# Kernel tuning notes

Measured on AMD Instinct MI355X. Metric: run time of the kernel, lower is better.

## Reference

```python
import jax, jax.numpy as jnp
import numpy as np

SAMPLE_RATE = 48000.0
WIN_SIZE = 512   # also the FFT size (nfft = win_size in forward)
HOP_SIZE = 256   # win_size // 2, COLA with Hann
B = 128
NUM_FREQ_PTS = 96000  # 2 s RIR at 48 kHz


def _hann(n):
    # torch.hann_window default is periodic: 0.5*(1 - cos(2*pi*k/n))
    k = jnp.arange(n, dtype=jnp.float32)
    return 0.5 * (1.0 - jnp.cos(2.0 * jnp.pi * k / n))


def _stft(x, win, nfft, hop):
    # x: [B, L] real. center=False, onesided=True, not normalized.
    L = x.shape[-1]
    pad = (-L) % hop  # pad to multiple of hop, as in get_stft_torch
    if pad:
        x = jnp.pad(x, ((0, 0), (0, pad)))
    T = (x.shape[-1] - nfft) // hop + 1  # number of frames
    idx = hop * jnp.arange(T)[:, None] + jnp.arange(nfft)[None, :]  # [T, nfft]
    frames = x[:, idx] * win  # [B, T, nfft]
    return jnp.fft.rfft(frames, n=nfft, axis=-1)  # [B, T, F], F = nfft//2 + 1


def _edr_db(S):
    # S: [B, T, F] complex. EDR[m] = sum_{t>=m} |S[t]|^2  -> reverse cumsum (O(T)).
    P = jnp.abs(S) ** 2  # [B, T, F]
    edr = jnp.flip(jnp.cumsum(jnp.flip(P, axis=1), axis=1), axis=1)
    return 10.0 * jnp.log10(edr)  # db(..., is_squared=True)


def reference(target_re, target_im, ach_re, ach_im):
    n = target_re.shape[-1]
    target_rir = jnp.fft.irfft(target_re + 1j * target_im, n=n)
    ach_rir = jnp.fft.irfft(ach_re + 1j * ach_im, n=n)
    win = _hann(WIN_SIZE)
    S_t = _stft(target_rir, win, WIN_SIZE, HOP_SIZE)
    S_a = _stft(ach_rir, win, WIN_SIZE, HOP_SIZE)
    edr_t = _edr_db(S_t)
    edr_a = _edr_db(S_a)
    return jnp.sum(jnp.abs(edr_t - edr_a)) / jnp.sum(jnp.abs(edr_t))


def setup_inputs() -> dict:
    key = jax.random.key(0)
    k1, k2, k3, k4 = jax.random.split(key, 4)
    shape = (B, NUM_FREQ_PTS)
    return {
        "target_re": jax.random.normal(k1, shape, dtype=jnp.float32),
        "target_im": jax.random.normal(k2, shape, dtype=jnp.float32),
        "ach_re": jax.random.normal(k3, shape, dtype=jnp.float32),
        "ach_im": jax.random.normal(k4, shape, dtype=jnp.float32),
    }
```

## Files before the change

### kernel.cpp

```cpp
#include <hip/hip_runtime.h>
#include <math.h>

#define BATCH   128
#define NFREQ   96000
#define M_HALF  48000
#define NFRAMES 374
#define NBINS   257
#define PPITCH  258
#define NG      11
#define GLEN    34
#define FPW     4

#define CS1 246
#define CS2 206

#define PI_D 3.14159265358979323846

#define WAVE_SYNC() __asm__ volatile("s_waitcnt lgkmcnt(0)" ::: "memory")

__device__ __forceinline__ float2 cmulf(float2 a, float2 b) {
  return make_float2(a.x * b.x - a.y * b.y, a.x * b.y + a.y * b.x);
}

__device__ __forceinline__ void bfly4(float2 z0, float2 z1, float2 z2, float2 z3,
                                      float2& o0, float2& o1, float2& o2, float2& o3) {
  float2 e0 = make_float2(z0.x + z2.x, z0.y + z2.y);
  float2 e1 = make_float2(z0.x - z2.x, z0.y - z2.y);
  float2 e2 = make_float2(z1.x + z3.x, z1.y + z3.y);
  float2 e3 = make_float2(z1.x - z3.x, z1.y - z3.y);
  o0 = make_float2(e0.x + e2.x, e0.y + e2.y);
  o2 = make_float2(e0.x - e2.x, e0.y - e2.y);
  o1 = make_float2(e1.x + e3.y, e1.y - e3.x);
  o3 = make_float2(e1.x - e3.y, e1.y + e3.x);
}

__device__ __forceinline__ void bfly4i(float2 z0, float2 z1, float2 z2, float2 z3,
                                       float2& o0, float2& o1, float2& o2, float2& o3) {
  float2 e0 = make_float2(z0.x + z2.x, z0.y + z2.y);
  float2 e1 = make_float2(z0.x - z2.x, z0.y - z2.y);
  float2 e2 = make_float2(z1.x + z3.x, z1.y + z3.y);
  float2 e3 = make_float2(z1.x - z3.x, z1.y - z3.y);
  o0 = make_float2(e0.x + e2.x, e0.y + e2.y);
  o2 = make_float2(e0.x - e2.x, e0.y - e2.y);
  o1 = make_float2(e1.x - e3.y, e1.y + e3.x);
  o3 = make_float2(e1.x + e3.y, e1.y - e3.x);
}

#define PIDX(i) ((i) + ((i) >> 3))

__global__ void setup_kernel(float2* __restrict__ Wm, float2* __restrict__ Wpack,
                             float2* __restrict__ W512, float* __restrict__ hann,
                             float2* __restrict__ W240, float2* __restrict__ W200) {
  int i = blockIdx.x * blockDim.x + threadIdx.x;
  if (i < M_HALF) {
    double th = 2.0 * PI_D * (double)i / (double)M_HALF;
    double s, c; sincos(th, &s, &c);
    Wm[i] = make_float2((float)c, (float)s);
    double th2 = PI_D * (double)i / (double)M_HALF;
    double s2, c2; sincos(th2, &s2, &c2);
    Wpack[i] = make_float2((float)c2, (float)s2);
  }
  if (i < 512) {
    double th = -2.0 * PI_D * (double)i / 512.0;
    double s, c; sincos(th, &s, &c);
    W512[i] = make_float2((float)c, (float)s);
    hann[i] = (float)(0.5 * (1.0 - cos(2.0 * PI_D * (double)i / 512.0)));
  }
  if (i < 240) {
    double th = 2.0 * PI_D * (double)i / 240.0;
    double s, c; sincos(th, &s, &c);
    W240[i] = make_float2((float)c, (float)s);
  }
  if (i < 200) {
    double th = 2.0 * PI_D * (double)i / 200.0;
    double s, c; sincos(th, &s, &c);
    W200[i] = make_float2((float)c, (float)s);
  }
}

__global__ __launch_bounds__(256) void packT_kernel(
    const float* __restrict__ tre, const float* __restrict__ tim,
    const float* __restrict__ are, const float* __restrict__ aim,
    float2* __restrict__ Zt, const float2* __restrict__ Wpack, int b0, int c) {
  __shared__ float4 dRe4[400], dIm4[400], mRe4[401], mIm4[401];
  float* dRe = (float*)dRe4;
  float* dIm = (float*)dIm4;
  float* mRe = (float*)mRe4;
  float* mIm = (float*)mIm4;
  const int tid = threadIdx.x;
  const int row = blockIdx.y;
  const int base = blockIdx.x * 1600;
  const int moff = M_HALF - base - 1600;
  const int isA = row >= c;
  const int b = b0 + (isA ? row - c : row);
  const float* rr = (isA ? are : tre) + (size_t)b * NFREQ;
  const float* ii = (isA ? aim : tim) + (size_t)b * NFREQ;
  {
    const float4* rd = (const float4*)(rr + base);
    const float4* id = (const float4*)(ii + base);
    for (int v = tid; v < 400; v += 256) { dRe4[v] = rd[v]; dIm4[v] = id[v]; }
    const float4* rm = (const float4*)(rr + moff);
    const float4* im = (const float4*)(ii + moff);
    for (int v = tid; v < 401; v += 256) { mRe4[v] = rm[v]; mIm4[v] = im[v]; }
  }
  __syncthreads();
  const float sc = 1.0f / (float)M_HALF;
  float2* Zrow = Zt + (size_t)row * M_HALF;
  const int k2base = blockIdx.x * 8;
  for (int e = tid; e < 800; e += 256) {
    int k1 = e >> 2, k2p = e & 3;
    float2 z[2];
#pragma unroll
    for (int h = 0; h < 2; ++h) {
      int j = k1 + 200 * (2 * k2p + h);
      int k = base + j;
      float xr = dRe[j], xi = dIm[j];
      float yr = mRe[1600 - j], yi = mIm[1600 - j];
      if (k == 0) { xi = 0.f; yi = 0.f; }
      float Er = 0.5f * (xr + yr);
      float Ei = 0.5f * (xi - yi);
      float Dr = 0.5f * (xr - yr);
      float Di = 0.5f * (xi + yi);
      float2 wp = Wpack[k];
      float tr = wp.x * Dr - wp.y * Di;
      float ti = wp.x * Di + wp.y * Dr;
      z[h] = make_float2((Er - ti) * sc, (Ei + tr) * sc);
    }
    ((float4*)Zrow)[k1 * 120 + (k2base >> 1) + k2p] =
        make_float4(z[0].x, z[0].y, z[1].x, z[1].y);
  }
}

__global__ __launch_bounds__(256) void k1_kernel(
    const float2* __restrict__ Zt, float2* __restrict__ G,
    const float2* __restrict__ Wm, const float2* __restrict__ W240) {
  __shared__ float2 LA[8 * CS1];
  __shared__ float2 LB[8 * CS1];
  const int tid = threadIdx.x;
  const int row = blockIdx.y;
  const int K0 = blockIdx.x * 8;

  {
    const float4* Zrow4 = (const float4*)(Zt + (size_t)row * M_HALF + (size_t)K0 * 240);
    for (int v = tid; v < 960; v += 256) {
      int col = v / 120;
      int k2 = 2 * (v - col * 120);
      *((float4*)(LA + col * CS1 + k2)) = Zrow4[v];
    }
  }
  __syncthreads();
  for (int e = tid; e < 8 * 60; e += 256) {
    int col = e & 7, p = e >> 3;
    const float2* in = LA + col * CS1;
    float2 o0, o1, o2, o3;
    bfly4i(in[p], in[p + 60], in[p + 120], in[p + 180], o0, o1, o2, o3);
    o1 = cmulf(o1, W240[p]);
    o2 = cmulf(o2, W240[2 * p]);
    o3 = cmulf(o3, W240[3 * p]);
    float2* out = LB + col * CS1 + 4 * p;
    out[0] = o0; out[1] = o1; out[2] = o2; out[3] = o3;
  }
  __syncthreads();
  for (int e = tid; e < 8 * 60; e += 256) {
    int col = e & 7, t = e >> 3;
    int q = t & 3, p = t >> 2;
    const float2* in = LB + col * CS1;
    float2 o0, o1, o2, o3;
    bfly4i(in[q + 4 * p], in[q + 4 * (p + 15)], in[q + 4 * (p + 30)],
           in[q + 4 * (p + 45)], o0, o1, o2, o3);
    o1 = cmulf(o1, W240[4 * p]);
    o2 = cmulf(o2, W240[8 * p]);
    o3 = cmulf(o3, W240[12 * p]);
    float2* out = LA + col * CS1 + q;
    out[4 * (4 * p + 0)] = o0; out[4 * (4 * p + 1)] = o1;
    out[4 * (4 * p + 2)] = o2; out[4 * (4 * p + 3)] = o3;
  }
  __syncthreads();
  {
    float2 w15[15];
#pragma unroll
    for (int m = 0; m < 15; ++m) w15[m] = W240[16 * m];
    for (int e = tid; e < 8 * 16; e += 256) {
      int col = e & 7, q = e >> 3;
      const float2* in = LA + col * CS1 + q;
      float2 a[15];
#pragma unroll
      for (int j = 0; j < 15; ++j) a[j] = in[16 * j];
      float2* out = LB + col * CS1 + q;
#pragma unroll
      for (int u = 0; u < 15; ++u) {
        float2 acc = a[0];
#pragma unroll
        for (int j = 1; j < 15; ++j) {
          float2 w = w15[(u * j) % 15];
          acc.x += a[j].x * w.x - a[j].y * w.y;
          acc.y += a[j].x * w.y + a[j].y * w.x;
        }
        out[16 * u] = acc;
      }
    }
  }
  __syncthreads();
  {
    const int cp = tid & 3;
    const int k1a = K0 + 2 * cp, k1b = k1a + 1;
    const int n2_0 = tid >> 2;
    float2 twa = Wm[k1a * n2_0];
    float2 twb = Wm[k1b * n2_0];
    const float2 sta = Wm[64 * k1a];
    const float2 stb = Wm[64 * k1b];
    float4* Grow4 = (float4*)(G + (size_t)row * M_HALF);
    const float2* ina = LB + (2 * cp) * CS1;
    const float2* inb = LB + (2 * cp + 1) * CS1;
    for (int n2 = n2_0; n2 < 240; n2 += 64) {
      float2 va = cmulf(ina[n2], twa);
      float2 vb = cmulf(inb[n2], twb);
      Grow4[n2 * 100 + (K0 >> 1) + cp] = make_float4(va.x, va.y, vb.x, vb.y);
      twa = cmulf(twa, sta);
      twb = cmulf(twb, stb);
    }
  }
}

__global__ __launch_bounds__(256) void k2_kernel(
    const float2* __restrict__ G, float2* __restrict__ X,
    const float2* __restrict__ W200) {
  __shared__ float2 LA[8 * CS2];
  __shared__ float2 LB[8 * CS2];
  const int tid = threadIdx.x;
  const int row = blockIdx.y;
  const int N20 = blockIdx.x * 8;

  {
    const float4* Grow4 = (const float4*)(G + (size_t)row * M_HALF + (size_t)N20 * 200);
    for (int v = tid; v < 800; v += 256) {
      int n2o = v / 100;
      int k1 = 2 * (v - n2o * 100);
      *((float4*)(LA + n2o * CS2 + k1)) = Grow4[v];
    }
  }
  __syncthreads();
  for (int e = tid; e < 8 * 50; e += 256) {
    int col = e & 7, p = e >> 3;
    const float2* in = LA + col * CS2;
    float2 o0, o1, o2, o3;
    bfly4i(in[p], in[p + 50], in[p + 100], in[p + 150], o0, o1, o2, o3);
    o1 = cmulf(o1, W200[p]);
    o2 = cmulf(o2, W200[2 * p]);
    o3 = cmulf(o3, W200[3 * p]);
    float2* out = LB + col * CS2 + 4 * p;
    out[0] = o0; out[1] = o1; out[2] = o2; out[3] = o3;
  }
  __syncthreads();
  {
    float2 w5[5];
#pragma unroll
    for (int m = 0; m < 5; ++m) w5[m] = W200[40 * m];
    for (int e = tid; e < 8 * 40; e += 256) {
      int col = e & 7, t = e >> 3;
      int q = t & 3, p = t >> 2;
      const float2* in = LB + col * CS2 + q;
      float2 a[5];
#pragma unroll
      for (int j = 0; j < 5; ++j) a[j] = in[4 * (p + 10 * j)];
      float2* out = LA + col * CS2 + q;
#pragma unroll
      for (int u = 0; u < 5; ++u) {
        float2 acc = a[0];
#pragma unroll
        for (int j = 1; j < 5; ++j) {
          float2 w = w5[(u * j) % 5];
          acc.x += a[j].x * w.x - a[j].y * w.y;
          acc.y += a[j].x * w.y + a[j].y * w.x;
        }
        acc = cmulf(acc, W200[4 * u * p]);
        out[4 * (5 * p + u)] = acc;
      }
    }
  }
  __syncthreads();
  {
    float2 w10[10];
#pragma unroll
    for (int m = 0; m < 10; ++m) w10[m] = W200[20 * m];
    for (int e = tid; e < 8 * 20; e += 256) {
      int col = e & 7, q = e >> 3;
      const float2* in = LA + col * CS2 + q;
      float2 a[10];
#pragma unroll
      for (int j = 0; j < 10; ++j) a[j] = in[20 * j];
      float2* out = LB + col * CS2 + q;
#pragma unroll
      for (int u = 0; u < 10; ++u) {
        float2 acc = a[0];
#pragma unroll
        for (int j = 1; j < 10; ++j) {
          float2 w = w10[(u * j) % 10];
          acc.x += a[j].x * w.x - a[j].y * w.y;
          acc.y += a[j].x * w.y + a[j].y * w.x;
        }
        out[20 * u] = acc;
      }
    }
  }
  __syncthreads();
  {
    const int np = tid & 3;
    const int n1_0 = tid >> 2;
    const float2* in0 = LB + (2 * np) * CS2;
    const float2* in1 = LB + (2 * np + 1) * CS2;
    float4* Xrow4 = (float4*)(X + (size_t)row * M_HALF);
    for (int n1 = n1_0; n1 < 200; n1 += 64) {
      float2 v0 = in0[n1], v1 = in1[n1];
      Xrow4[(N20 >> 1) + np + 120 * n1] = make_float4(v0.x, v0.y, v1.x, v1.y);
    }
  }
}

__global__ __launch_bounds__(256) void stft256_kernel(
    const float* __restrict__ xtime, float* __restrict__ P,
    float* __restrict__ part,
    const float2* __restrict__ W512, const float* __restrict__ hann) {
  __shared__ float2 lds[4][2][288];
  const int tid = threadIdx.x;
  const int wave = tid >> 6;
  const int l = tid & 63;
  const int row = blockIdx.y;
  const int frame0 = (blockIdx.x * 4 + wave) * FPW;

  float2* Abuf = lds[wave][0];
  float2* Bbuf = lds[wave][1];

  const float4 hh0 = ((const float4*)hann)[l];
  const float4 hh1 = ((const float4*)hann)[l + 64];
  float2 t1[3], t2[3], t3[3];
  {
    int p2 = l >> 2, p3 = l >> 4;
#pragma unroll
    for (int u = 1; u <= 3; ++u) {
      t1[u - 1] = W512[2 * u * l];
      t2[u - 1] = W512[8 * u * p2];
      t3[u - 1] = W512[32 * u * p3];
    }
  }

  const float2* xrow = (const float2*)xtime + (size_t)row * 48000;
  float acc[5] = {0.f, 0.f, 0.f, 0.f, 0.f};

  for (int fi = 0; fi < FPW; ++fi) {
    const int fr = frame0 + fi;
    if (fr >= NFRAMES) break;
    {
      const float4* src4 = (const float4*)(xrow + fr * 128);
      float4 v0 = src4[l];
      float4 v1 = src4[l + 64];
      v0.x *= hh0.x; v0.y *= hh0.y; v0.z *= hh0.z; v0.w *= hh0.w;
      v1.x *= hh1.x; v1.y *= hh1.y; v1.z *= hh1.z; v1.w *= hh1.w;
      ((float4*)Bbuf)[l] = v0;
      ((float4*)Bbuf)[l + 64] = v1;
    }
    WAVE_SYNC();
    float2 o0, o1, o2, o3;
    {
      float2 z0 = Bbuf[l], z1 = Bbuf[l + 64], z2 = Bbuf[l + 128], z3 = Bbuf[l + 192];
      bfly4(z0, z1, z2, z3, o0, o1, o2, o3);
      o1 = cmulf(o1, t1[0]); o2 = cmulf(o2, t1[1]); o3 = cmulf(o3, t1[2]);
      Abuf[PIDX(4 * l + 0)] = o0; Abuf[PIDX(4 * l + 1)] = o1;
      Abuf[PIDX(4 * l + 2)] = o2; Abuf[PIDX(4 * l + 3)] = o3;
    }
    WAVE_SYNC();
    {
      int q = l & 3, p = l >> 2;
      float2 a0 = Abuf[PIDX(q + 4 * p)];
      float2 a1 = Abuf[PIDX(q + 4 * (p + 16))];
      float2 a2 = Abuf[PIDX(q + 4 * (p + 32))];
      float2 a3 = Abuf[PIDX(q + 4 * (p + 48))];
      bfly4(a0, a1, a2, a3, o0, o1, o2, o3);
      o1 = cmulf(o1, t2[0]); o2 = cmulf(o2, t2[1]); o3 = cmulf(o3, t2[2]);
      int wb = q + 16 * p;
      Bbuf[PIDX(wb)] = o0; Bbuf[PIDX(wb + 4)] = o1;
      Bbuf[PIDX(wb + 8)] = o2; Bbuf[PIDX(wb + 12)] = o3;
    }
    WAVE_SYNC();
    {
      int q = l & 15, p = l >> 4;
      float2 a0 = Bbuf[PIDX(q + 16 * p)];
      float2 a1 = Bbuf[PIDX(q + 16 * (p + 4))];
      float2 a2 = Bbuf[PIDX(q + 16 * (p + 8))];
      float2 a3 = Bbuf[PIDX(q + 16 * (p + 12))];
      bfly4(a0, a1, a2, a3, o0, o1, o2, o3);
      o1 = cmulf(o1, t3[0]); o2 = cmulf(o2, t3[1]); o3 = cmulf(o3, t3[2]);
      int wb = q + 64 * p;
      Abuf[PIDX(wb)] = o0; Abuf[PIDX(wb + 16)] = o1;
      Abuf[PIDX(wb + 32)] = o2; Abuf[PIDX(wb + 48)] = o3;
    }
    WAVE_SYNC();
    {
      float2 a0 = Abuf[PIDX(l)];
      float2 a1 = Abuf[PIDX(l + 64)];
      float2 a2 = Abuf[PIDX(l + 128)];
      float2 a3 = Abuf[PIDX(l + 192)];
      bfly4(a0, a1, a2, a3, o0, o1, o2, o3);
      Bbuf[PIDX(l)] = o0; Bbuf[PIDX(l + 64)] = o1;
      Bbuf[PIDX(l + 128)] = o2; Bbuf[PIDX(l + 192)] = o3;
    }
    WAVE_SYNC();
    {
      float* Prow = P + ((size_t)row * NFRAMES + fr) * PPITCH;
      int j = 0;
      for (int k = l; k <= 256; k += 64, ++j) {
        float2 Zk = Bbuf[PIDX(k & 255)];
        float2 Zm = Bbuf[PIDX((256 - k) & 255)];
        float2 E  = make_float2(0.5f * (Zk.x + Zm.x), 0.5f * (Zk.y - Zm.y));
        float2 Op = make_float2(Zk.x - Zm.x, Zk.y + Zm.y);
        float2 Od = make_float2(0.5f * Op.y, -0.5f * Op.x);
        float2 W  = W512[k];
        float2 Xb = make_float2(E.x + W.x * Od.x - W.y * Od.y,
                                E.y + W.x * Od.y + W.y * Od.x);
        float pwr = Xb.x * Xb.x + Xb.y * Xb.y;
        Prow[k] = pwr;
        acc[j] += pwr;
      }
      bool flush = (((fr + 1) % GLEN) == 0) || (fi == FPW - 1) || (fr == NFRAMES - 1);
      if (flush) {
        int g = fr / GLEN;
        float* prow = part + ((size_t)row * NG + g) * PPITCH;
        int j2 = 0;
        for (int k = l; k <= 256; k += 64, ++j2) {
          atomicAdd(&prow[k], acc[j2]);
          acc[j2] = 0.f;
        }
      }
    }
    WAVE_SYNC();
  }
}

__global__ __launch_bounds__(192) void edrB_kernel(const float* __restrict__ P,
                                                   const float* __restrict__ part,
                                                   double* __restrict__ accum, int c) {
  const int b = blockIdx.x;
  const int g = blockIdx.y;
  const int tid = threadIdx.x;
  const float* Pt = P + (size_t)b * (NFRAMES * PPITCH);
  const float* Pa = P + (size_t)(b + c) * (NFRAMES * PPITCH);
  const float* qt = part + (size_t)b * NG * PPITCH;
  const float* qa = part + (size_t)(b + c) * NG * PPITCH;
  float sn = 0.f, sd = 0.f;
  if (tid < 128) {
    const int bin = 2 * tid;
    float2 ct = make_float2(0.f, 0.f), ca = make_float2(0.f, 0.f);
    for (int g2 = g + 1; g2 < NG; ++g2) {
      float2 vt = *(const float2*)(qt + g2 * PPITCH + bin);
      float2 va = *(const float2*)(qa + g2 * PPITCH + bin);
      ct.x += vt.x; ct.y += vt.y; ca.x += va.x; ca.y += va.y;
    }
    const int m0 = g * GLEN;
    for (int m = m0 + GLEN - 1; m >= m0; --m) {
      float2 vt = *(const float2*)(Pt + m * PPITCH + bin);
      float2 va = *(const float2*)(Pa + m * PPITCH + bin);
      ct.x += vt.x; ct.y += vt.y; ca.x += va.x; ca.y += va.y;
      float lt0 = 10.f * log10f(ct.x), la0 = 10.f * log10f(ca.x);
      float lt1 = 10.f * log10f(ct.y), la1 = 10.f * log10f(ca.y);
      sn += fabsf(lt0 - la0) + fabsf(lt1 - la1);
      sd += fabsf(lt0) + fabsf(lt1);
    }
  } else if (tid == 128) {
    const int bin = 256;
    float ct = 0.f, ca = 0.f;
    for (int g2 = g + 1; g2 < NG; ++g2) {
      ct += qt[g2 * PPITCH + bin];
      ca += qa[g2 * PPITCH + bin];
    }
    const int m0 = g * GLEN;
    for (int m = m0 + GLEN - 1; m >= m0; --m) {
      ct += Pt[m * PPITCH + bin];
      ca += Pa[m * PPITCH + bin];
      float lt = 10.f * log10f(ct), la = 10.f * log10f(ca);
      sn += fabsf(lt - la);
      sd += fabsf(lt);
    }
  }
#pragma unroll
  for (int off = 32; off > 0; off >>= 1) {
    sn += __shfl_down(sn, off, 64);
    sd += __shfl_down(sd, off, 64);
  }
  __shared__ float wsn[3], wsd[3];
  const int wave = tid >> 6;
  if ((tid & 63) == 0) { wsn[wave] = sn; wsd[wave] = sd; }
  __syncthreads();
  if (tid == 0) {
    float tn = 0.f, td = 0.f;
#pragma unroll
    for (int w = 0; w < 3; ++w) { tn += wsn[w]; td += wsd[w]; }
    int slot = (blockIdx.x * NG + blockIdx.y) & 63;
    atomicAdd(&accum[slot], (double)tn);
    atomicAdd(&accum[64 + slot], (double)td);
  }
}

__global__ void final_kernel(const double* __restrict__ accum, float* __restrict__ out) {
  double n = 0.0, d = 0.0;
  for (int i = 0; i < 64; ++i) { n += accum[i]; d += accum[64 + i]; }
  out[0] = (float)(n / d);
}

extern "C" void kernel_launch(void* const* d_in, const int* in_sizes, int n_in,
                              void* d_out, int out_size, void* d_ws, size_t ws_size,
                              hipStream_t stream) {
  const float* tre = (const float*)d_in[0];
  const float* tim = (const float*)d_in[1];
  const float* are = (const float*)d_in[2];
  const float* aim = (const float*)d_in[3];
  float* out = (float*)d_out;

  char* base = (char*)d_ws;
  size_t off = 0;
  auto take = [&](size_t bytes) -> char* {
    char* p = base + off;
    off += (bytes + 255) & ~(size_t)255;
    return p;
  };
  float2* Wm    = (float2*)take((size_t)M_HALF * sizeof(float2));
  float2* Wpack = (float2*)take((size_t)M_HALF * sizeof(float2));
  float2* W512  = (float2*)take(512 * sizeof(float2));
  float*  hann  = (float*)take(512 * sizeof(float));
  float2* W240  = (float2*)take(240 * sizeof(float2));
  float2* W200  = (float2*)take(200 * sizeof(float2));
  double* accum = (double*)take(128 * sizeof(double));
  size_t fixed = off;

  const size_t perA    = (size_t)2 * M_HALF * sizeof(float2);
  const size_t perP    = (size_t)2 * NFRAMES * PPITCH * sizeof(float);
  const size_t perPart = (size_t)2 * NG * PPITCH * sizeof(float);
  int c = 1;
  const int cands[8] = {128, 64, 32, 16, 8, 4, 2, 1};
  for (int ci = 0; ci < 8; ++ci) {
    size_t need = fixed + ((cands[ci] * perA + 255) & ~(size_t)255)
                        + ((cands[ci] * perP + 255) & ~(size_t)255)
                        + ((cands[ci] * perPart + 255) & ~(size_t)255);
    if (need <= ws_size) { c = cands[ci]; break; }
  }
  float2* buf1 = (float2*)take((size_t)c * perA);
  char*   BP   = take((size_t)c * perP);
  float*  part = (float*)take((size_t)c * perPart);
  float2* Zt = buf1;
  float2* X  = buf1;
  float2* G  = (float2*)BP;
  float*  P  = (float*)BP;

  setup_kernel<<<(M_HALF + 255) / 256, 256, 0, stream>>>(Wm, Wpack, W512, hann,
                                                         W240, W200);
  hipMemsetAsync(accum, 0, 128 * sizeof(double), stream);

  for (int b0 = 0; b0 < BATCH; b0 += c) {
    int rows = 2 * c;
    hipMemsetAsync(part, 0, (size_t)c * perPart, stream);
    packT_kernel<<<dim3(30, rows), 256, 0, stream>>>(tre, tim, are, aim, Zt,
                                                     Wpack, b0, c);
    k1_kernel<<<dim3(25, rows), 256, 0, stream>>>(Zt, G, Wm, W240);
    k2_kernel<<<dim3(30, rows), 256, 0, stream>>>(G, X, W200);
    {
      dim3 grid((NFRAMES + 4 * FPW - 1) / (4 * FPW), rows);
      stft256_kernel<<<grid, 256, 0, stream>>>((const float*)X, P, part, W512, hann);
    }
    edrB_kernel<<<dim3(c, NG), 192, 0, stream>>>(P, part, accum, c);
  }
  final_kernel<<<1, 1, 0, stream>>>(accum, out);
}
```

Measured before the change: 415.9 us.

## Factor pack twiddles, prefetch next STFT frame, shrink EDR block to 128 threads

The 48000-entry Wpack twiddle table is replaced by two small tables (200 and 240 entries) whose product is formed per element in packT, which cuts table traffic and the double-precision sincos work in setup. The STFT kernel now loads the next frame's samples into registers while the current frame is processed, to hide global load latency. The EDR kernel drops its third, mostly idle wave and has thread 127 handle the Nyquist bin. In exchange there is one extra complex multiply per element and a small change in twiddle rounding, plus higher register pressure in the STFT kernel.

```diff
diff --git a/kernel.cpp b/kernel.cpp
--- a/kernel.cpp
+++ b/kernel.cpp
@@ -48,17 +48,15 @@
 
 #define PIDX(i) ((i) + ((i) >> 3))
 
-__global__ void setup_kernel(float2* __restrict__ Wm, float2* __restrict__ Wpack,
+__global__ void setup_kernel(float2* __restrict__ Wm,
                              float2* __restrict__ W512, float* __restrict__ hann,
-                             float2* __restrict__ W240, float2* __restrict__ W200) {
+                             float2* __restrict__ W240, float2* __restrict__ W200,
+                             float2* __restrict__ Wp200a, float2* __restrict__ Wp240b) {
   int i = blockIdx.x * blockDim.x + threadIdx.x;
   if (i < M_HALF) {
     double th = 2.0 * PI_D * (double)i / (double)M_HALF;
     double s, c; sincos(th, &s, &c);
     Wm[i] = make_float2((float)c, (float)s);
-    double th2 = PI_D * (double)i / (double)M_HALF;
-    double s2, c2; sincos(th2, &s2, &c2);
-    Wpack[i] = make_float2((float)c2, (float)s2);
   }
   if (i < 512) {
     double th = -2.0 * PI_D * (double)i / 512.0;
@@ -70,18 +68,25 @@
     double th = 2.0 * PI_D * (double)i / 240.0;
     double s, c; sincos(th, &s, &c);
     W240[i] = make_float2((float)c, (float)s);
+    double thb = PI_D * (double)i / 240.0;
+    double sb, cb; sincos(thb, &sb, &cb);
+    Wp240b[i] = make_float2((float)cb, (float)sb);
   }
   if (i < 200) {
     double th = 2.0 * PI_D * (double)i / 200.0;
     double s, c; sincos(th, &s, &c);
     W200[i] = make_float2((float)c, (float)s);
+    double tha = PI_D * (double)i / (double)M_HALF;
+    double sa, ca; sincos(tha, &sa, &ca);
+    Wp200a[i] = make_float2((float)ca, (float)sa);
   }
 }
 
 __global__ __launch_bounds__(256) void packT_kernel(
     const float* __restrict__ tre, const float* __restrict__ tim,
     const float* __restrict__ are, const float* __restrict__ aim,
-    float2* __restrict__ Zt, const float2* __restrict__ Wpack, int b0, int c) {
+    float2* __restrict__ Zt, const float2* __restrict__ Wp200a,
+    const float2* __restrict__ Wp240b, int b0, int c) {
   __shared__ float4 dRe4[400], dIm4[400], mRe4[401], mIm4[401];
   float* dRe = (float*)dRe4;
   float* dIm = (float*)dIm4;
@@ -95,6 +100,10 @@
   const int b = b0 + (isA ? row - c : row);
   const float* rr = (isA ? are : tre) + (size_t)b * NFREQ;
   const float* ii = (isA ? aim : tim) + (size_t)b * NFREQ;
+  const int k2base = blockIdx.x * 8;
+  float2 Bt[8];
+#pragma unroll
+  for (int h8 = 0; h8 < 8; ++h8) Bt[h8] = Wp240b[k2base + h8];
   {
     const float4* rd = (const float4*)(rr + base);
     const float4* id = (const float4*)(ii + base);
@@ -106,9 +115,9 @@
   __syncthreads();
   const float sc = 1.0f / (float)M_HALF;
   float2* Zrow = Zt + (size_t)row * M_HALF;
-  const int k2base = blockIdx.x * 8;
   for (int e = tid; e < 800; e += 256) {
     int k1 = e >> 2, k2p = e & 3;
+    float2 Ak = Wp200a[k1];
     float2 z[2];
 #pragma unroll
     for (int h = 0; h < 2; ++h) {
@@ -121,7 +130,7 @@
       float Ei = 0.5f * (xi - yi);
       float Dr = 0.5f * (xr - yr);
       float Di = 0.5f * (xi + yi);
-      float2 wp = Wpack[k];
+      float2 wp = cmulf(Ak, Bt[2 * k2p + h]);
       float tr = wp.x * Dr - wp.y * Di;
       float ti = wp.x * Di + wp.y * Dr;
       z[h] = make_float2((Er - ti) * sc, (Ei + tr) * sc);
@@ -344,16 +353,27 @@
     }
   }
 
-  const float2* xrow = (const float2*)xtime + (size_t)row * 48000;
+  const float4* base4 = (const float4*)((const float2*)xtime + (size_t)row * 48000);
   float acc[5] = {0.f, 0.f, 0.f, 0.f, 0.f};
+
+  float4 c0 = make_float4(0.f, 0.f, 0.f, 0.f);
+  float4 c1 = c0;
+  if (frame0 < NFRAMES) {
+    c0 = base4[frame0 * 64 + l];
+    c1 = base4[frame0 * 64 + 64 + l];
+  }
 
   for (int fi = 0; fi < FPW; ++fi) {
     const int fr = frame0 + fi;
     if (fr >= NFRAMES) break;
-    {
-      const float4* src4 = (const float4*)(xrow + fr * 128);
-      float4 v0 = src4[l];
-      float4 v1 = src4[l + 64];
+    float4 n0 = make_float4(0.f, 0.f, 0.f, 0.f);
+    float4 n1 = n0;
+    if (fi + 1 < FPW && fr + 1 < NFRAMES) {
+      n0 = base4[(fr + 1) * 64 + l];
+      n1 = base4[(fr + 1) * 64 + 64 + l];
+    }
+    {
+      float4 v0 = c0, v1 = c1;
       v0.x *= hh0.x; v0.y *= hh0.y; v0.z *= hh0.z; v0.w *= hh0.w;
       v1.x *= hh1.x; v1.y *= hh1.y; v1.z *= hh1.z; v1.w *= hh1.w;
       ((float4*)Bbuf)[l] = v0;
@@ -433,10 +453,11 @@
       }
     }
     WAVE_SYNC();
-  }
-}
-
-__global__ __launch_bounds__(192) void edrB_kernel(const float* __restrict__ P,
+    c0 = n0; c1 = n1;
+  }
+}
+
+__global__ __launch_bounds__(128) void edrB_kernel(const float* __restrict__ P,
                                                    const float* __restrict__ part,
                                                    double* __restrict__ accum, int c) {
   const int b = blockIdx.x;
@@ -447,13 +468,15 @@
   const float* qt = part + (size_t)b * NG * PPITCH;
   const float* qa = part + (size_t)(b + c) * NG * PPITCH;
   float sn = 0.f, sd = 0.f;
-  if (tid < 128) {
+  {
     const int bin = 2 * tid;
     float2 ct = make_float2(0.f, 0.f), ca = make_float2(0.f, 0.f);
+    float ct2 = 0.f, ca2 = 0.f;
     for (int g2 = g + 1; g2 < NG; ++g2) {
       float2 vt = *(const float2*)(qt + g2 * PPITCH + bin);
       float2 va = *(const float2*)(qa + g2 * PPITCH + bin);
       ct.x += vt.x; ct.y += vt.y; ca.x += va.x; ca.y += va.y;
+      if (tid == 127) { ct2 += qt[g2 * PPITCH + 256]; ca2 += qa[g2 * PPITCH + 256]; }
     }
     const int m0 = g * GLEN;
     for (int m = m0 + GLEN - 1; m >= m0; --m) {
@@ -464,21 +487,13 @@
       float lt1 = 10.f * log10f(ct.y), la1 = 10.f * log10f(ca.y);
       sn += fabsf(lt0 - la0) + fabsf(lt1 - la1);
       sd += fabsf(lt0) + fabsf(lt1);
-    }
-  } else if (tid == 128) {
-    const int bin = 256;
-    float ct = 0.f, ca = 0.f;
-    for (int g2 = g + 1; g2 < NG; ++g2) {
-      ct += qt[g2 * PPITCH + bin];
-      ca += qa[g2 * PPITCH + bin];
-    }
-    const int m0 = g * GLEN;
-    for (int m = m0 + GLEN - 1; m >= m0; --m) {
-      ct += Pt[m * PPITCH + bin];
-      ca += Pa[m * PPITCH + bin];
-      float lt = 10.f * log10f(ct), la = 10.f * log10f(ca);
-      sn += fabsf(lt - la);
-      sd += fabsf(lt);
+      if (tid == 127) {
+        ct2 += Pt[m * PPITCH + 256];
+        ca2 += Pa[m * PPITCH + 256];
+        float lt = 10.f * log10f(ct2), la = 10.f * log10f(ca2);
+        sn += fabsf(lt - la);
+        sd += fabsf(lt);
+      }
     }
   }
 #pragma unroll
@@ -486,14 +501,13 @@
     sn += __shfl_down(sn, off, 64);
     sd += __shfl_down(sd, off, 64);
   }
-  __shared__ float wsn[3], wsd[3];
+  __shared__ float wsn[2], wsd[2];
   const int wave = tid >> 6;
   if ((tid & 63) == 0) { wsn[wave] = sn; wsd[wave] = sd; }
   __syncthreads();
   if (tid == 0) {
-    float tn = 0.f, td = 0.f;
-#pragma unroll
-    for (int w = 0; w < 3; ++w) { tn += wsn[w]; td += wsd[w]; }
+    float tn = wsn[0] + wsn[1];
+    float td = wsd[0] + wsd[1];
     int slot = (blockIdx.x * NG + blockIdx.y) & 63;
     atomicAdd(&accum[slot], (double)tn);
     atomicAdd(&accum[64 + slot], (double)td);
@@ -522,13 +536,14 @@
     off += (bytes + 255) & ~(size_t)255;
     return p;
   };
-  float2* Wm    = (float2*)take((size_t)M_HALF * sizeof(float2));
-  float2* Wpack = (float2*)take((size_t)M_HALF * sizeof(float2));
-  float2* W512  = (float2*)take(512 * sizeof(float2));
-  float*  hann  = (float*)take(512 * sizeof(float));
-  float2* W240  = (float2*)take(240 * sizeof(float2));
-  float2* W200  = (float2*)take(200 * sizeof(float2));
-  double* accum = (double*)take(128 * sizeof(double));
+  float2* Wm     = (float2*)take((size_t)M_HALF * sizeof(float2));
+  float2* W512   = (float2*)take(512 * sizeof(float2));
+  float*  hann   = (float*)take(512 * sizeof(float));
+  float2* W240   = (float2*)take(240 * sizeof(float2));
+  float2* W200   = (float2*)take(200 * sizeof(float2));
+  float2* Wp200a = (float2*)take(200 * sizeof(float2));
+  float2* Wp240b = (float2*)take(240 * sizeof(float2));
+  double* accum  = (double*)take(128 * sizeof(double));
   size_t fixed = off;
 
   const size_t perA    = (size_t)2 * M_HALF * sizeof(float2);
@@ -550,22 +565,22 @@
   float2* G  = (float2*)BP;
   float*  P  = (float*)BP;
 
-  setup_kernel<<<(M_HALF + 255) / 256, 256, 0, stream>>>(Wm, Wpack, W512, hann,
-                                                         W240, W200);
+  setup_kernel<<<(M_HALF + 255) / 256, 256, 0, stream>>>(Wm, W512, hann,
+                                                         W240, W200, Wp200a, Wp240b);
   hipMemsetAsync(accum, 0, 128 * sizeof(double), stream);
 
   for (int b0 = 0; b0 < BATCH; b0 += c) {
     int rows = 2 * c;
     hipMemsetAsync(part, 0, (size_t)c * perPart, stream);
     packT_kernel<<<dim3(30, rows), 256, 0, stream>>>(tre, tim, are, aim, Zt,
-                                                     Wpack, b0, c);
+                                                     Wp200a, Wp240b, b0, c);
     k1_kernel<<<dim3(25, rows), 256, 0, stream>>>(Zt, G, Wm, W240);
     k2_kernel<<<dim3(30, rows), 256, 0, stream>>>(G, X, W200);
     {
       dim3 grid((NFRAMES + 4 * FPW - 1) / (4 * FPW), rows);
       stft256_kernel<<<grid, 256, 0, stream>>>((const float*)X, P, part, W512, hann);
     }
-    edrB_kernel<<<dim3(c, NG), 192, 0, stream>>>(P, part, accum, c);
+    edrB_kernel<<<dim3(c, NG), 128, 0, stream>>>(P, part, accum, c);
   }
   final_kernel<<<1, 1, 0, stream>>>(accum, out);
 }
```

Result: slower. 446.4 us (+7.3%).
